# Optimization experiments

Measured on AMD Instinct MI355X. Metric: run time of the kernel, lower is better.

The kernel has to match this reference:

```python
import jax, jax.numpy as jnp
import numpy as np

R_CUT = 10.0  # init arg r_cut


def _per_mol(pos, T, eneg, node_attrs, an, q_tot, eidx, hardness, cov_radii):
    # pos [N,3], T [N,E], eneg [N], node_attrs [N,num_el], an [N] int,
    # q_tot scalar, eidx [2,E] int
    N = pos.shape[0]
    E = T.shape[1]
    dtype = pos.dtype
    sqrt_pi = jnp.sqrt(jnp.pi).astype(dtype)
    sqrt_2 = jnp.sqrt(2.0).astype(dtype)
    eye = jnp.eye(N, dtype=dtype)
    # pairwise distances; +eye makes the (masked-out) diagonal sqrt-safe
    diff = pos[:, None, :] - pos[None, :, :]
    d = jnp.sqrt(jnp.sum(diff * diff, axis=-1) + eye)  # [N,N]
    r = cov_radii[an]                                   # [N]
    sigma = r * r
    gamma = jnp.sqrt(sigma[:, None] + sigma[None, :])   # [N,N]
    diag_vals = hardness[jnp.argmax(node_attrs, axis=-1)] + 1.0 / (sqrt_pi * r)
    A = jax.scipy.special.erf(d / (sqrt_2 * gamma)) / d * (1.0 - eye) + jnp.diag(diag_vals)
    # per-edge cutoff diagonal: 1/cos(pi*r/(2*r_cut)) - 1
    e0, e1 = eidx[0], eidx[1]
    edge_d = jnp.sqrt(jnp.sum((pos[e0] - pos[e1]) ** 2, axis=-1))  # [E]
    cut = 1.0 / jnp.cos(jnp.pi * edge_d / (2.0 * R_CUT)) - 1.0
    Ap = T.T @ A @ T + jnp.diag(cut)                    # [E,E]
    # augment with charge-conservation row/col of ones
    ones_col = jnp.ones((E, 1), dtype=dtype)
    ones_row = jnp.ones((1, E + 1), dtype=dtype)
    Aaug = jnp.concatenate([jnp.concatenate([Ap, ones_col], axis=1), ones_row], axis=0)
    b = jnp.concatenate([-(T.T @ eneg), q_tot[None]])   # [E+1]
    x = jnp.linalg.solve(Aaug, b)[:-1]                  # [E] split charges
    return T @ x                                        # [N] atomic partial charges


def setup_inputs() -> dict:
    key = jax.random.key(0)
    B, N, E, NUM_EL, NZ = 256, 64, 512, 10, 119
    ks = jax.random.split(key, 10)
    positions = jax.random.normal(ks[0], (B, N, 3), dtype=jnp.float32)
    T = jax.random.normal(ks[1], (B, N, E), dtype=jnp.float32)
    eneg = jax.random.normal(ks[2], (B, N), dtype=jnp.float32)
    node_attrs = jax.random.normal(ks[3], (B, N, NUM_EL), dtype=jnp.float32)
    total_charge = jax.random.normal(ks[4], (B,), dtype=jnp.float32)
    atomic_numbers = jax.random.randint(ks[5], (B, N), 1, 100)
    e0 = jax.random.randint(ks[6], (B, E), 0, N)
    off = jax.random.randint(ks[7], (B, E), 1, N)
    edge_index = jnp.stack([e0, (e0 + off) % N], axis=1)  # [B,2,E], distinct endpoints
    hardness = jax.random.uniform(ks[8], (NUM_EL,), dtype=jnp.float32)
    cov_radii = 0.3 + 2.2 * jax.random.uniform(ks[9], (NZ,), dtype=jnp.float32)
    p = jnp.zeros((1,), dtype=jnp.float32)  # only used for .device in torch
    return dict(positions=positions, T=T, eneg=eneg, node_attrs=node_attrs,
                total_charge=total_charge, p=p, hardness=hardness,
                cov_radii=cov_radii, atomic_numbers=atomic_numbers,
                edge_index=edge_index)


def reference(positions, T, eneg, node_attrs, total_charge, p, hardness,
              cov_radii, atomic_numbers, edge_index):
    charges = jax.vmap(_per_mol, in_axes=(0, 0, 0, 0, 0, 0, 0, None, None))(
        positions, T, eneg, node_attrs, atomic_numbers, total_charge,
        edge_index, hardness, cov_radii)  # [B,N]
    return charges.reshape(-1)  # concat over molecules, as in the torch loop
```

## Files before the change

kernel.cpp:

```cpp
#include <hip/hip_runtime.h>
#include <math.h>

#define SQRT_PI 1.7724538509055160273
#define SQRT_2  1.4142135623730950488
#define PI_OVER_2RC 0.15707963267948966
#define W0 32.0

typedef double dbl4 __attribute__((ext_vector_type(4)));


__device__ __forceinline__ double bcast64(double v, int lane) {
    union { double d; unsigned int u[2]; } a, r;
    a.d = v;
    r.u[0] = __builtin_amdgcn_readlane(a.u[0], lane);
    r.u[1] = __builtin_amdgcn_readlane(a.u[1], lane);
    return r.d;
}

__device__ __forceinline__ double a_entry(int i, int j, const double* posd,
                                          const double* sig, const double* dg) {
    if (i == j) return dg[i];
    double dx = posd[3*i+0]-posd[3*j+0];
    double dy = posd[3*i+1]-posd[3*j+1];
    double dz = posd[3*i+2]-posd[3*j+2];
    double d  = sqrt(dx*dx+dy*dy+dz*dz);
    double g  = sqrt(sig[i]+sig[j]);
    return erf(d/(SQRT_2*g))/d;
}

__device__ __forceinline__ dbl4 mfma64(int cS, double xv, double yv, dbl4 acc) {
    return cS ? __builtin_amdgcn_mfma_f64_16x16x4f64(yv, xv, acc, 0, 0, 0)
              : __builtin_amdgcn_mfma_f64_16x16x4f64(xv, yv, acc, 0, 0, 0);
}

__global__ __launch_bounds__(64)
void k0_probe(double* __restrict__ fl)
{
    const int l = threadIdx.x;
    const int kl = l >> 4, ml = l & 15;
    const double af1 = (double)(l + 1),  bf1 = (double)(l + 65);
    const double af2 = (double)(1 + ((l*7 + 3) % 61));
    const double bf2 = (double)(2 + ((l*13 + 5) % 53));
    dbl4 c1 = {0.0,0.0,0.0,0.0}, c2 = {0.0,0.0,0.0,0.0};
    c1 = __builtin_amdgcn_mfma_f64_16x16x4f64(af1, bf1, c1, 0, 0, 0);
    c2 = __builtin_amdgcn_mfma_f64_16x16x4f64(af2, bf2, c2, 0, 0, 0);
    int best = -1;
    for (int h = 0; h < 32; ++h) {
        if (best >= 0) break;
        const int cS = h >> 4, cA = (h >> 3) & 1, cB = (h >> 2) & 1, cD = h & 3;
        bool ok = true;
        #pragma unroll
        for (int r = 0; r < 4; ++r) {
            int row, col;
            const int v0 = 4*kl + r, v1 = kl + 4*r;
            if (cD == 0)      { row = v0; col = ml; }
            else if (cD == 1) { row = v1; col = ml; }
            else if (cD == 2) { row = ml; col = v0; }
            else              { row = ml; col = v1; }
            double r1 = 0.0, r2 = 0.0;
            #pragma unroll
            for (int k = 0; k < 4; ++k) {
                const int la = cA ? (row*4 + k) : (row + 16*k);
                const int lb = cB ? (col*4 + k) : (col + 16*k);
                if (cS == 0) {
                    r1 += (double)(la + 1) * (double)(lb + 65);
                    r2 += (double)(1 + ((la*7+3) % 61)) * (double)(2 + ((lb*13+5) % 53));
                } else {
                    r1 += (double)(lb + 1) * (double)(la + 65);
                    r2 += (double)(1 + ((lb*7+3) % 61)) * (double)(2 + ((la*13+5) % 53));
                }
            }
            if (c1[r] != r1 || c2[r] != r2) ok = false;
        }
        if (__ballot(ok) == ~0ull) best = h;
    }
    if (l == 0) {
        fl[0] = (best >= 0) ? 1.0 : 0.0;
        fl[1] = (double)((best >= 0) ? (best >> 4)      : 0);
        fl[2] = (double)((best >= 0) ? ((best >> 3) & 1) : 0);
        fl[3] = (double)((best >= 0) ? ((best >> 2) & 1) : 0);
        fl[4] = (double)((best >= 0) ? (best & 3)        : 0);
    }
}

__global__ __launch_bounds__(256, 2)
void k1_gram(const float* __restrict__ pos, const float* __restrict__ T,
             const int* __restrict__ eidx, double* __restrict__ ws)
{
    const int bx = blockIdx.x;
    const int m = bx >> 1, s = bx & 1;
    const int Bm = gridDim.x >> 1;
    const int tid = threadIdx.x;
    const int wid = tid >> 6, l = tid & 63;
    const int kl = l >> 4, ml = l & 15;

    __shared__ float  Tch[64*68];
    __shared__ double posd[192];
    __shared__ double w_sl[256];
    __shared__ float  sw32[256];
    __shared__ double ptb[4][64];
    __shared__ unsigned long long fmask[4];

    const float* Tm = T + (size_t)m*64*512;
    const double* flq = ws + (size_t)Bm*8322;
    const int useM = (flq[0] != 0.0);
    const int cS = (int)flq[1], cA = (int)flq[2], cB = (int)flq[3], cD = (int)flq[4];
    const int aRow = cA ? (l >> 2) : ml;
    const int aK   = cA ? (l & 3)  : kl;
    const int bRow = cB ? (l >> 2) : ml;
    const int bK   = cB ? (l & 3)  : kl;
    int drow[4], dcol[4];
    #pragma unroll
    for (int r = 0; r < 4; ++r) {
        const int v0 = 4*kl + r, v1 = kl + 4*r;
        if (cD == 0)      { drow[r] = v0; dcol[r] = ml; }
        else if (cD == 1) { drow[r] = v1; dcol[r] = ml; }
        else if (cD == 2) { drow[r] = ml; dcol[r] = v0; }
        else              { drow[r] = ml; dcol[r] = v1; }
    }

    if (tid < 64) {
        posd[3*tid+0] = (double)pos[(m*64+tid)*3+0];
        posd[3*tid+1] = (double)pos[(m*64+tid)*3+1];
        posd[3*tid+2] = (double)pos[(m*64+tid)*3+2];
    }
    __syncthreads();

    {
        const int e = s*256 + tid;
        const int a0 = eidx[(size_t)m*1024 + e];
        const int a1 = eidx[(size_t)m*1024 + 512 + e];
        double dx = posd[3*a0+0]-posd[3*a1+0];
        double dy = posd[3*a0+1]-posd[3*a1+1];
        double dz = posd[3*a0+2]-posd[3*a1+2];
        double d  = sqrt(dx*dx+dy*dy+dz*dz);
        double w  = 1.0 / (1.0/cos(PI_OVER_2RC*d) - 1.0);
        w_sl[tid] = w;
        sw32[tid] = (w > W0) ? 0.0f : (float)sqrt(w);
    }
    __syncthreads();
    if (tid < 64) {
        #pragma unroll
        for (int c2 = 0; c2 < 4; ++c2) {
            unsigned long long mk = __ballot(w_sl[c2*64 + tid] > W0);
            if (tid == 0) fmask[c2] = mk;
        }
    }

    const int si = tid & 15, sj = tid >> 4;
    const int ti64 = tid & 63, tg = tid >> 6;

    const unsigned int enc = (wid==0) ? 0x020100u :
                             (wid==1) ? 0x121103u :
                             (wid==2) ? 0xFF2213u : 0xFF3323u;
    dbl4 vacc[3];
    #pragma unroll
    for (int t = 0; t < 3; ++t) vacc[t] = (dbl4){0.0, 0.0, 0.0, 0.0};

    const int PP_[10] = {0,0,0,0,1,1,1,2,2,3};
    const int QQ_[10] = {0,1,2,3,1,2,3,2,3,3};
    double acc64[10];
    float  a32[10];
    #pragma unroll
    for (int k = 0; k < 10; ++k) { acc64[k] = 0.0; a32[k] = 0.0f; }
    double t0b_p = 0.0;

    for (int cc = 0; cc < 4; ++cc) {
        const int gch = s*4 + cc;
        __syncthreads();
        #pragma unroll
        for (int k = 0; k < 4; ++k) {
            int ll = tid + 256*k, row = ll >> 4, c4 = (ll & 15)*4;
            float4 v = *(const float4*)&Tm[row*512 + gch*64 + c4];
            *(float4*)&Tch[row*68 + c4] = v;
        }
        __syncthreads();
        #pragma unroll
        for (int k = 0; k < 16; ++k) {
            int e = tg*16 + k;
            double tv = (double)Tch[ti64*68 + e];
            t0b_p += tv * w_sl[cc*64 + e];
        }
        if (useM) {
            for (int kk = 0; kk < 16; ++kk) {
                const double wB = w_sl[cc*64 + 4*kk + bK];
                #pragma unroll
                for (int t = 0; t < 3; ++t) {
                    const unsigned int pq = (enc >> (8*t)) & 0xFFu;
                    if (pq != 0xFFu) {
                        const int p = pq >> 4, q = pq & 15;
                        double xv = (double)Tch[(p*16 + aRow)*68 + 4*kk + aK];
                        double yv = wB * (double)Tch[(q*16 + bRow)*68 + 4*kk + bK];
                        vacc[t] = mfma64(cS, xv, yv, vacc[t]);
                    }
                }
            }
        } else {
            {
                unsigned long long mm = fmask[cc];
                while (mm) {
                    int e = __builtin_ctzll(mm); mm &= mm - 1;
                    double we = w_sl[cc*64 + e];
                    double ad[4], bd[4];
                    #pragma unroll
                    for (int p = 0; p < 4; ++p) ad[p] = (double)Tch[(si+16*p)*68 + e];
                    #pragma unroll
                    for (int q = 0; q < 4; ++q) bd[q] = we * (double)Tch[(sj+16*q)*68 + e];
                    #pragma unroll
                    for (int k = 0; k < 10; ++k) acc64[k] += ad[PP_[k]] * bd[QQ_[k]];
                }
            }
            __syncthreads();
            #pragma unroll
            for (int k = 0; k < 4; ++k) {
                int ll = tid + 256*k, row = ll >> 4, c4 = (ll & 15)*4;
                float4 v = *(float4*)&Tch[row*68 + c4];
                v.x *= sw32[cc*64 + c4+0];
                v.y *= sw32[cc*64 + c4+1];
                v.z *= sw32[cc*64 + c4+2];
                v.w *= sw32[cc*64 + c4+3];
                *(float4*)&Tch[row*68 + c4] = v;
            }
            __syncthreads();
            #pragma unroll
            for (int e4 = 0; e4 < 16; ++e4) {
                float4 av4[4], bv4[4];
                #pragma unroll
                for (int p = 0; p < 4; ++p) av4[p] = *(float4*)&Tch[(si+16*p)*68 + e4*4];
                #pragma unroll
                for (int q = 0; q < 4; ++q) bv4[q] = *(float4*)&Tch[(sj+16*q)*68 + e4*4];
                #pragma unroll
                for (int k = 0; k < 10; ++k) {
                    const float4 a4 = av4[PP_[k]], b4 = bv4[QQ_[k]];
                    a32[k] += a4.x*b4.x + a4.y*b4.y + a4.z*b4.z + a4.w*b4.w;
                }
                if ((e4 & 3) == 3) {
                    #pragma unroll
                    for (int k = 0; k < 10; ++k) { acc64[k] += (double)a32[k]; a32[k] = 0.0f; }
                }
            }
        }
    }
    __syncthreads();

    double* Sp = ws + ((size_t)(s*Bm + m))*4096;
    if (useM) {
        #pragma unroll
        for (int t = 0; t < 3; ++t) {
            const unsigned int pq = (enc >> (8*t)) & 0xFFu;
            if (pq != 0xFFu) {
                const int p = pq >> 4, q = pq & 15;
                #pragma unroll
                for (int r = 0; r < 4; ++r) {
                    Sp[(p*16 + drow[r])*64 + q*16 + dcol[r]] = vacc[t][r];
                    if (p != q)
                        Sp[(q*16 + dcol[r])*64 + p*16 + drow[r]] = vacc[t][r];
                }
            }
        }
    } else {
        #pragma unroll
        for (int k = 0; k < 10; ++k) {
            int i = si + 16*PP_[k], j = sj + 16*QQ_[k];
            Sp[i*64 + j] = acc64[k];
            if (PP_[k] != QQ_[k]) Sp[j*64 + i] = acc64[k];
        }
    }

    ptb[tg][ti64] = t0b_p;
    __syncthreads();
    if (tid < 64) {
        double* t0q = ws + (size_t)2*Bm*4096;
        t0q[(size_t)(s*Bm + m)*64 + tid] =
            ptb[0][tid]+ptb[1][tid]+ptb[2][tid]+ptb[3][tid];
        double sw = w_sl[tid] + w_sl[64+tid] + w_sl[128+tid] + w_sl[192+tid];
        #pragma unroll
        for (int off = 32; off > 0; off >>= 1) sw += __shfl_down(sw, off);
        if (tid == 0) {
            double* swq = ws + (size_t)2*Bm*4096 + (size_t)2*Bm*64;
            swq[s*Bm + m] = sw;
        }
    }
}

__global__ __launch_bounds__(1024)
void k2_solve(const float* __restrict__ pos, const float* __restrict__ nattr,
              const float* __restrict__ eneg, const float* __restrict__ qtot,
              const float* __restrict__ hard, const float* __restrict__ covr,
              const int* __restrict__ an, double* __restrict__ ws,
              float* __restrict__ outp)
{
    const int m = blockIdx.x, tid = threadIdx.x;
    const int Bm = gridDim.x;
    const int jl = tid & 63;
    const int rg = tid >> 6;
    const int kl = jl >> 4, ml = jl & 15;

    __shared__ double AB[64*65];
    __shared__ double PB[64*33];
    __shared__ double posd[192], sig_s[64], dg_s[64], eneg_s[64];
    __shared__ double t0a_s[64], t0b_s[64], ga_s[64], gb_s[64], ua_s[64], ub_s[64];
    __shared__ double sa_s[64], sb_s[64];
    __shared__ double dinv_s[64], dvec_s[64];
    __shared__ double lam_sh;

    const double* Sp0 = ws + (size_t)m*4096;
    const double* Sp1 = ws + (size_t)(Bm + m)*4096;
    const double* t0q = ws + (size_t)2*Bm*4096;
    const double* swq = t0q + (size_t)2*Bm*64;
    const double* flq = ws + (size_t)Bm*8322;

    const int useM = (flq[0] != 0.0);
    const int cS = (int)flq[1], cA = (int)flq[2], cB = (int)flq[3], cD = (int)flq[4];
    const int aRow = cA ? (jl >> 2) : ml;
    const int aK   = cA ? (jl & 3)  : kl;
    const int bRow = cB ? (jl >> 2) : ml;
    const int bK   = cB ? (jl & 3)  : kl;
    int drow[4], dcol[4];
    #pragma unroll
    for (int r = 0; r < 4; ++r) {
        const int v0 = 4*kl + r, v1 = kl + 4*r;
        if (cD == 0)      { drow[r] = v0; dcol[r] = ml; }
        else if (cD == 1) { drow[r] = v1; dcol[r] = ml; }
        else if (cD == 2) { drow[r] = ml; dcol[r] = v0; }
        else              { drow[r] = ml; dcol[r] = v1; }
    }

    double sreg[4];
    #pragma unroll
    for (int kk = 0; kk < 4; ++kk)
        sreg[kk] = Sp0[4*tid + kk] + Sp1[4*tid + kk];

    if (tid < 64) {
        posd[3*tid+0] = (double)pos[(m*64+tid)*3+0];
        posd[3*tid+1] = (double)pos[(m*64+tid)*3+1];
        posd[3*tid+2] = (double)pos[(m*64+tid)*3+2];
        double r = (double)covr[an[m*64+tid]];
        sig_s[tid] = r*r;
        const float* np_ = nattr + (size_t)(m*64+tid)*10;
        float best = np_[0]; int bi = 0;
        #pragma unroll
        for (int k = 1; k < 10; ++k) { float v = np_[k]; if (v > best) { best = v; bi = k; } }
        dg_s[tid] = (double)hard[bi] + 1.0/(SQRT_PI*r);
    } else if (tid < 128) {
        int ll = tid - 64;
        t0b_s[ll] = t0q[(size_t)m*64 + ll] + t0q[(size_t)(Bm+m)*64 + ll];
    } else if (tid < 192) {
        int ll = tid - 128;
        eneg_s[ll] = (double)eneg[m*64 + ll];
    }
    __syncthreads();

    double areg[4];
    #pragma unroll
    for (int p = 0; p < 4; ++p) {
        int i = rg + 16*p;
        double v = a_entry(i, jl, posd, sig_s, dg_s);
        areg[p] = v;
        AB[i*65 + jl] = v;
    }
    {
        const int c16 = tid & 15, row16 = tid >> 4;
        double a = 0.0;
        #pragma unroll
        for (int kk = 0; kk < 4; ++kk) a += sreg[kk] * eneg_s[4*c16 + kk];
        a += __shfl_down(a, 8, 16);
        a += __shfl_down(a, 4, 16);
        a += __shfl_down(a, 2, 16);
        a += __shfl_down(a, 1, 16);
        if (c16 == 0) t0a_s[row16] = -a;
    }
    __syncthreads();

    {
        double ra[4], rb[4];
        const double ta = t0a_s[jl], tb = t0b_s[jl];
        #pragma unroll
        for (int p = 0; p < 4; ++p) { ra[p] = areg[p]*ta; rb[p] = areg[p]*tb; }
        #pragma unroll
        for (int off = 32; off > 0; off >>= 1) {
            #pragma unroll
            for (int p = 0; p < 4; ++p) {
                ra[p] += __shfl_down(ra[p], off);
                rb[p] += __shfl_down(rb[p], off);
            }
        }
        if (jl == 0) {
            #pragma unroll
            for (int p = 0; p < 4; ++p) { ga_s[rg+16*p] = ra[p]; gb_s[rg+16*p] = rb[p]; }
        }
    }
    __syncthreads();

    if (useM) {
        const int ti1 = rg >> 2;
        const int tjp = (rg & 3) >> 1;
        const int kh  = rg & 1;
        const int ti2 = rg >> 2, tj2 = rg & 3;
        dbl4 macc;
        #pragma unroll
        for (int r = 0; r < 4; ++r)
            macc[r] = AB[(ti2*16 + drow[r])*65 + tj2*16 + dcol[r]];
        for (int pass = 0; pass < 2; ++pass) {
            const int kbase = pass*32;
            dbl4 pacc = {0.0, 0.0, 0.0, 0.0};
            #pragma unroll
            for (int kk = 0; kk < 8; ++kk) {
                const int kg = kh*8 + kk;
                double xv = AB[(ti1*16 + aRow)*65 + 4*kg + aK];
                size_t so = (size_t)(4*kg + bK)*64 + kbase + tjp*16 + bRow;
                double yv = Sp0[so] + Sp1[so];
                pacc = mfma64(cS, xv, yv, pacc);
            }
            __syncthreads();
            if (kh == 0) {
                #pragma unroll
                for (int r = 0; r < 4; ++r)
                    PB[(ti1*16 + drow[r])*33 + tjp*16 + dcol[r]] = pacc[r];
            }
            __syncthreads();
            if (kh == 1) {
                #pragma unroll
                for (int r = 0; r < 4; ++r)
                    PB[(ti1*16 + drow[r])*33 + tjp*16 + dcol[r]] += pacc[r];
            }
            __syncthreads();
            #pragma unroll
            for (int kk = 0; kk < 8; ++kk) {
                double xv = PB[(ti2*16 + aRow)*33 + 4*kk + aK];
                double yv = AB[(kbase + 4*kk + bK)*65 + tj2*16 + bRow];
                macc = mfma64(cS, xv, yv, macc);
            }
        }
        __syncthreads();
        #pragma unroll
        for (int r = 0; r < 4; ++r)
            AB[(ti2*16 + drow[r])*65 + tj2*16 + dcol[r]] = macc[r];
        __syncthreads();
    } else {
        double macc[4];
        #pragma unroll
        for (int p = 0; p < 4; ++p) macc[p] = areg[p];
        for (int pass = 0; pass < 2; ++pass) {
            const int kbase = pass*32;
            __syncthreads();
            for (int l2 = tid; l2 < 2048; l2 += 1024) {
                int c = l2 >> 6, k = l2 & 63;
                PB[c*64 + k] = Sp0[(size_t)(kbase+c)*64 + k] + Sp1[(size_t)(kbase+c)*64 + k];
            }
            __syncthreads();
            const int c0 = 2*rg, c1 = c0 + 1;
            double p0 = 0.0, p1 = 0.0;
            #pragma unroll 4
            for (int k = 0; k < 64; ++k) {
                double a = AB[jl*65 + k];
                p0 += a * PB[c0*64 + k];
                p1 += a * PB[c1*64 + k];
            }
            __syncthreads();
            PB[jl*33 + c0] = p0;
            PB[jl*33 + c1] = p1;
            __syncthreads();
            #pragma unroll 4
            for (int cl = 0; cl < 32; ++cl) {
                double lb = AB[(kbase+cl)*65 + jl];
                #pragma unroll
                for (int p = 0; p < 4; ++p)
                    macc[p] += PB[(rg+16*p)*33 + cl] * lb;
            }
        }
        __syncthreads();
        #pragma unroll
        for (int p = 0; p < 4; ++p) AB[(rg+16*p)*65 + jl] = macc[p];
        __syncthreads();
    }

    for (int pb = 0; pb < 4; ++pb) {
        const int kb = pb*16;
        if (tid < 64) {
            const int i = tid;
            double pr[16];
            #pragma unroll
            for (int c = 0; c < 16; ++c) pr[c] = AB[i*65 + kb + c];
            #pragma unroll
            for (int c = 0; c < 16; ++c) {
                const int k = kb + c;
                const double Dk = bcast64(pr[c], k);
                const double di = 1.0 / Dk;
                if (i == k) { dinv_s[k] = di; dvec_s[k] = Dk; }
                const double lik = pr[c] * di;
                #pragma unroll
                for (int j = c+1; j < 16; ++j) {
                    const double mkj = bcast64(pr[j], k);
                    if (i > k) pr[j] -= lik * mkj;
                }
                if (i > k) pr[c] = lik;
            }
            #pragma unroll
            for (int c = 0; c < 16; ++c) AB[i*65 + kb + c] = pr[c];
        }
        __syncthreads();
        const int lim = kb + 16;
        if (lim < 64) {
            double tacc[4] = {0.0, 0.0, 0.0, 0.0};
            #pragma unroll 4
            for (int c = 0; c < 16; ++c) {
                double lbv = AB[jl*65 + kb + c] * dvec_s[kb + c];
                #pragma unroll
                for (int p = 0; p < 4; ++p)
                    tacc[p] += AB[(rg+16*p)*65 + kb + c] * lbv;
            }
            if (jl >= lim) {
                #pragma unroll
                for (int p = 0; p < 4; ++p) {
                    int i = rg + 16*p;
                    if (i >= lim) AB[i*65 + jl] -= tacc[p];
                }
            }
        }
        __syncthreads();
    }

    if (tid < 64) {
        const int i = tid;
        double ha = ga_s[i], hb = gb_s[i];
        #pragma unroll
        for (int j = 0; j < 63; ++j) {
            double xa = bcast64(ha, j), xb = bcast64(hb, j);
            double lij = (i > j) ? AB[i*65+j] : 0.0;
            ha -= lij*xa; hb -= lij*xb;
        }
        double di = dinv_s[i];
        ha *= di; hb *= di;
        #pragma unroll
        for (int j = 63; j > 0; --j) {
            double xa = bcast64(ha, j), xb = bcast64(hb, j);
            double lji = (i < j) ? AB[j*65+i] : 0.0;
            ha -= lji*xa; hb -= lji*xb;
        }
        ua_s[i] = ha; ub_s[i] = hb;
    }
    __syncthreads();

    {
        double ra[4], rb[4];
        const double uaj = ua_s[jl], ubj = ub_s[jl];
        #pragma unroll
        for (int p = 0; p < 4; ++p) { ra[p] = areg[p]*uaj; rb[p] = areg[p]*ubj; }
        #pragma unroll
        for (int off = 32; off > 0; off >>= 1) {
            #pragma unroll
            for (int p = 0; p < 4; ++p) {
                ra[p] += __shfl_down(ra[p], off);
                rb[p] += __shfl_down(rb[p], off);
            }
        }
        if (jl == 0) {
            #pragma unroll
            for (int p = 0; p < 4; ++p) {
                sa_s[rg + 16*p] = ra[p];
                sb_s[rg + 16*p] = rb[p];
            }
        }
    }
    __syncthreads();

    {
        const int c16 = tid & 15, row16 = tid >> 4;
        double q1 = 0.0, q2 = 0.0;
        #pragma unroll
        for (int kk = 0; kk < 4; ++kk) {
            q1 += sreg[kk] * sa_s[4*c16 + kk];
            q2 += sreg[kk] * sb_s[4*c16 + kk];
        }
        q1 += __shfl_down(q1, 8, 16); q2 += __shfl_down(q2, 8, 16);
        q1 += __shfl_down(q1, 4, 16); q2 += __shfl_down(q2, 4, 16);
        q1 += __shfl_down(q1, 2, 16); q2 += __shfl_down(q2, 2, 16);
        q1 += __shfl_down(q1, 1, 16); q2 += __shfl_down(q2, 1, 16);
        if (c16 == 0) { PB[row16] = q1; PB[64 + row16] = q2; }
    }
    if (tid < 64) {
        double d1 = (eneg_s[tid] + sa_s[tid]) * t0b_s[tid];
        double d2 = sb_s[tid] * t0b_s[tid];
        #pragma unroll
        for (int off = 32; off > 0; off >>= 1) {
            d1 += __shfl_down(d1, off);
            d2 += __shfl_down(d2, off);
        }
        if (tid == 0) {
            double sw1 = swq[m] + swq[Bm + m];
            double sY = -d1;
            double sZ = sw1 - d2;
            lam_sh = ((double)qtot[m] - sY) / (1.0 - sZ);
        }
    }
    __syncthreads();
    if (tid < 64) {
        double p1 = t0a_s[tid] - PB[tid];
        double p2 = t0b_s[tid] - PB[64 + tid];
        outp[m*64 + tid] = (float)(p1 - lam_sh*p2);
    }
}

extern "C" void kernel_launch(void* const* d_in, const int* in_sizes, int n_in,
                              void* d_out, int out_size, void* d_ws, size_t ws_size,
                              hipStream_t stream) {
    const float* pos  = (const float*)d_in[0];
    const float* T    = (const float*)d_in[1];
    const float* eneg = (const float*)d_in[2];
    const float* nat  = (const float*)d_in[3];
    const float* qt   = (const float*)d_in[4];
    const float* hard = (const float*)d_in[6];
    const float* covr = (const float*)d_in[7];
    const int*   an   = (const int*)d_in[8];
    const int*   eidx = (const int*)d_in[9];
    float* outp = (float*)d_out;
    (void)n_in; (void)out_size; (void)ws_size;

    const int B = in_sizes[4];
    double* ws = (double*)d_ws;

    k0_probe<<<dim3(1), dim3(64), 0, stream>>>(ws + (size_t)B*8322);
    k1_gram<<<dim3(2*B), dim3(256), 0, stream>>>(pos, T, eidx, ws);
    k2_solve<<<dim3(B), dim3(1024), 0, stream>>>(pos, nat, eneg, qt, hard,
                                                 covr, an, ws, outp);
}
```

Measured before the change: 181.3 us.

## Fuse Gram kernel into solve kernel, keeping the weighted Gram matrix in LDS

Result: slower. 195.6 us (+7.9%).

```diff
diff --git a/kernel.cpp b/kernel.cpp
--- a/kernel.cpp
+++ b/kernel.cpp
@@ -4,7 +4,6 @@
 #define SQRT_PI 1.7724538509055160273
 #define SQRT_2  1.4142135623730950488
 #define PI_OVER_2RC 0.15707963267948966
-#define W0 32.0
 
 typedef double dbl4 __attribute__((ext_vector_type(4)));
 
@@ -83,234 +82,31 @@
     }
 }
 
-__global__ __launch_bounds__(256, 2)
-void k1_gram(const float* __restrict__ pos, const float* __restrict__ T,
-             const int* __restrict__ eidx, double* __restrict__ ws)
-{
-    const int bx = blockIdx.x;
-    const int m = bx >> 1, s = bx & 1;
-    const int Bm = gridDim.x >> 1;
-    const int tid = threadIdx.x;
-    const int wid = tid >> 6, l = tid & 63;
-    const int kl = l >> 4, ml = l & 15;
-
-    __shared__ float  Tch[64*68];
-    __shared__ double posd[192];
-    __shared__ double w_sl[256];
-    __shared__ float  sw32[256];
-    __shared__ double ptb[4][64];
-    __shared__ unsigned long long fmask[4];
-
-    const float* Tm = T + (size_t)m*64*512;
-    const double* flq = ws + (size_t)Bm*8322;
-    const int useM = (flq[0] != 0.0);
-    const int cS = (int)flq[1], cA = (int)flq[2], cB = (int)flq[3], cD = (int)flq[4];
-    const int aRow = cA ? (l >> 2) : ml;
-    const int aK   = cA ? (l & 3)  : kl;
-    const int bRow = cB ? (l >> 2) : ml;
-    const int bK   = cB ? (l & 3)  : kl;
-    int drow[4], dcol[4];
-    #pragma unroll
-    for (int r = 0; r < 4; ++r) {
-        const int v0 = 4*kl + r, v1 = kl + 4*r;
-        if (cD == 0)      { drow[r] = v0; dcol[r] = ml; }
-        else if (cD == 1) { drow[r] = v1; dcol[r] = ml; }
-        else if (cD == 2) { drow[r] = ml; dcol[r] = v0; }
-        else              { drow[r] = ml; dcol[r] = v1; }
-    }
-
-    if (tid < 64) {
-        posd[3*tid+0] = (double)pos[(m*64+tid)*3+0];
-        posd[3*tid+1] = (double)pos[(m*64+tid)*3+1];
-        posd[3*tid+2] = (double)pos[(m*64+tid)*3+2];
-    }
-    __syncthreads();
-
-    {
-        const int e = s*256 + tid;
-        const int a0 = eidx[(size_t)m*1024 + e];
-        const int a1 = eidx[(size_t)m*1024 + 512 + e];
-        double dx = posd[3*a0+0]-posd[3*a1+0];
-        double dy = posd[3*a0+1]-posd[3*a1+1];
-        double dz = posd[3*a0+2]-posd[3*a1+2];
-        double d  = sqrt(dx*dx+dy*dy+dz*dz);
-        double w  = 1.0 / (1.0/cos(PI_OVER_2RC*d) - 1.0);
-        w_sl[tid] = w;
-        sw32[tid] = (w > W0) ? 0.0f : (float)sqrt(w);
-    }
-    __syncthreads();
-    if (tid < 64) {
-        #pragma unroll
-        for (int c2 = 0; c2 < 4; ++c2) {
-            unsigned long long mk = __ballot(w_sl[c2*64 + tid] > W0);
-            if (tid == 0) fmask[c2] = mk;
-        }
-    }
-
-    const int si = tid & 15, sj = tid >> 4;
-    const int ti64 = tid & 63, tg = tid >> 6;
-
-    const unsigned int enc = (wid==0) ? 0x020100u :
-                             (wid==1) ? 0x121103u :
-                             (wid==2) ? 0xFF2213u : 0xFF3323u;
-    dbl4 vacc[3];
-    #pragma unroll
-    for (int t = 0; t < 3; ++t) vacc[t] = (dbl4){0.0, 0.0, 0.0, 0.0};
-
-    const int PP_[10] = {0,0,0,0,1,1,1,2,2,3};
-    const int QQ_[10] = {0,1,2,3,1,2,3,2,3,3};
-    double acc64[10];
-    float  a32[10];
-    #pragma unroll
-    for (int k = 0; k < 10; ++k) { acc64[k] = 0.0; a32[k] = 0.0f; }
-    double t0b_p = 0.0;
-
-    for (int cc = 0; cc < 4; ++cc) {
-        const int gch = s*4 + cc;
-        __syncthreads();
-        #pragma unroll
-        for (int k = 0; k < 4; ++k) {
-            int ll = tid + 256*k, row = ll >> 4, c4 = (ll & 15)*4;
-            float4 v = *(const float4*)&Tm[row*512 + gch*64 + c4];
-            *(float4*)&Tch[row*68 + c4] = v;
-        }
-        __syncthreads();
-        #pragma unroll
-        for (int k = 0; k < 16; ++k) {
-            int e = tg*16 + k;
-            double tv = (double)Tch[ti64*68 + e];
-            t0b_p += tv * w_sl[cc*64 + e];
-        }
-        if (useM) {
-            for (int kk = 0; kk < 16; ++kk) {
-                const double wB = w_sl[cc*64 + 4*kk + bK];
-                #pragma unroll
-                for (int t = 0; t < 3; ++t) {
-                    const unsigned int pq = (enc >> (8*t)) & 0xFFu;
-                    if (pq != 0xFFu) {
-                        const int p = pq >> 4, q = pq & 15;
-                        double xv = (double)Tch[(p*16 + aRow)*68 + 4*kk + aK];
-                        double yv = wB * (double)Tch[(q*16 + bRow)*68 + 4*kk + bK];
-                        vacc[t] = mfma64(cS, xv, yv, vacc[t]);
-                    }
-                }
-            }
-        } else {
-            {
-                unsigned long long mm = fmask[cc];
-                while (mm) {
-                    int e = __builtin_ctzll(mm); mm &= mm - 1;
-                    double we = w_sl[cc*64 + e];
-                    double ad[4], bd[4];
-                    #pragma unroll
-                    for (int p = 0; p < 4; ++p) ad[p] = (double)Tch[(si+16*p)*68 + e];
-                    #pragma unroll
-                    for (int q = 0; q < 4; ++q) bd[q] = we * (double)Tch[(sj+16*q)*68 + e];
-                    #pragma unroll
-                    for (int k = 0; k < 10; ++k) acc64[k] += ad[PP_[k]] * bd[QQ_[k]];
-                }
-            }
-            __syncthreads();
-            #pragma unroll
-            for (int k = 0; k < 4; ++k) {
-                int ll = tid + 256*k, row = ll >> 4, c4 = (ll & 15)*4;
-                float4 v = *(float4*)&Tch[row*68 + c4];
-                v.x *= sw32[cc*64 + c4+0];
-                v.y *= sw32[cc*64 + c4+1];
-                v.z *= sw32[cc*64 + c4+2];
-                v.w *= sw32[cc*64 + c4+3];
-                *(float4*)&Tch[row*68 + c4] = v;
-            }
-            __syncthreads();
-            #pragma unroll
-            for (int e4 = 0; e4 < 16; ++e4) {
-                float4 av4[4], bv4[4];
-                #pragma unroll
-                for (int p = 0; p < 4; ++p) av4[p] = *(float4*)&Tch[(si+16*p)*68 + e4*4];
-                #pragma unroll
-                for (int q = 0; q < 4; ++q) bv4[q] = *(float4*)&Tch[(sj+16*q)*68 + e4*4];
-                #pragma unroll
-                for (int k = 0; k < 10; ++k) {
-                    const float4 a4 = av4[PP_[k]], b4 = bv4[QQ_[k]];
-                    a32[k] += a4.x*b4.x + a4.y*b4.y + a4.z*b4.z + a4.w*b4.w;
-                }
-                if ((e4 & 3) == 3) {
-                    #pragma unroll
-                    for (int k = 0; k < 10; ++k) { acc64[k] += (double)a32[k]; a32[k] = 0.0f; }
-                }
-            }
-        }
-    }
-    __syncthreads();
-
-    double* Sp = ws + ((size_t)(s*Bm + m))*4096;
-    if (useM) {
-        #pragma unroll
-        for (int t = 0; t < 3; ++t) {
-            const unsigned int pq = (enc >> (8*t)) & 0xFFu;
-            if (pq != 0xFFu) {
-                const int p = pq >> 4, q = pq & 15;
-                #pragma unroll
-                for (int r = 0; r < 4; ++r) {
-                    Sp[(p*16 + drow[r])*64 + q*16 + dcol[r]] = vacc[t][r];
-                    if (p != q)
-                        Sp[(q*16 + dcol[r])*64 + p*16 + drow[r]] = vacc[t][r];
-                }
-            }
-        }
-    } else {
-        #pragma unroll
-        for (int k = 0; k < 10; ++k) {
-            int i = si + 16*PP_[k], j = sj + 16*QQ_[k];
-            Sp[i*64 + j] = acc64[k];
-            if (PP_[k] != QQ_[k]) Sp[j*64 + i] = acc64[k];
-        }
-    }
-
-    ptb[tg][ti64] = t0b_p;
-    __syncthreads();
-    if (tid < 64) {
-        double* t0q = ws + (size_t)2*Bm*4096;
-        t0q[(size_t)(s*Bm + m)*64 + tid] =
-            ptb[0][tid]+ptb[1][tid]+ptb[2][tid]+ptb[3][tid];
-        double sw = w_sl[tid] + w_sl[64+tid] + w_sl[128+tid] + w_sl[192+tid];
-        #pragma unroll
-        for (int off = 32; off > 0; off >>= 1) sw += __shfl_down(sw, off);
-        if (tid == 0) {
-            double* swq = ws + (size_t)2*Bm*4096 + (size_t)2*Bm*64;
-            swq[s*Bm + m] = sw;
-        }
-    }
-}
-
 __global__ __launch_bounds__(1024)
-void k2_solve(const float* __restrict__ pos, const float* __restrict__ nattr,
-              const float* __restrict__ eneg, const float* __restrict__ qtot,
-              const float* __restrict__ hard, const float* __restrict__ covr,
-              const int* __restrict__ an, double* __restrict__ ws,
-              float* __restrict__ outp)
+void k_fused(const float* __restrict__ pos, const float* __restrict__ T,
+             const int* __restrict__ eidx, const float* __restrict__ nattr,
+             const float* __restrict__ eneg, const float* __restrict__ qtot,
+             const float* __restrict__ hard, const float* __restrict__ covr,
+             const int* __restrict__ an, const double* __restrict__ flq,
+             float* __restrict__ outp)
 {
     const int m = blockIdx.x, tid = threadIdx.x;
-    const int Bm = gridDim.x;
     const int jl = tid & 63;
     const int rg = tid >> 6;
     const int kl = jl >> 4, ml = jl & 15;
 
     __shared__ double AB[64*65];
-    __shared__ double PB[64*33];
+    __shared__ double SB[64*65];
+    __shared__ union {
+        struct { float Tch[64*68]; double w_sl[512]; } g;
+        double PF[64*65];
+    } U;
     __shared__ double posd[192], sig_s[64], dg_s[64], eneg_s[64];
-    __shared__ double t0a_s[64], t0b_s[64], ga_s[64], gb_s[64], ua_s[64], ub_s[64];
-    __shared__ double sa_s[64], sb_s[64];
+    __shared__ double t0a_s[64], t0b_s[64], ga_s[64], gb_s[64];
+    __shared__ double ua_s[64], ub_s[64], sa_s[64], sb_s[64];
     __shared__ double dinv_s[64], dvec_s[64];
-    __shared__ double lam_sh;
-
-    const double* Sp0 = ws + (size_t)m*4096;
-    const double* Sp1 = ws + (size_t)(Bm + m)*4096;
-    const double* t0q = ws + (size_t)2*Bm*4096;
-    const double* swq = t0q + (size_t)2*Bm*64;
-    const double* flq = ws + (size_t)Bm*8322;
-
-    const int useM = (flq[0] != 0.0);
+    __shared__ double lam_sh, sw_sh;
+
     const int cS = (int)flq[1], cA = (int)flq[2], cB = (int)flq[3], cD = (int)flq[4];
     const int aRow = cA ? (jl >> 2) : ml;
     const int aK   = cA ? (jl & 3)  : kl;
@@ -326,11 +122,6 @@
         else              { drow[r] = ml; dcol[r] = v1; }
     }
 
-    double sreg[4];
-    #pragma unroll
-    for (int kk = 0; kk < 4; ++kk)
-        sreg[kk] = Sp0[4*tid + kk] + Sp1[4*tid + kk];
-
     if (tid < 64) {
         posd[3*tid+0] = (double)pos[(m*64+tid)*3+0];
         posd[3*tid+1] = (double)pos[(m*64+tid)*3+1];
@@ -344,13 +135,19 @@
         dg_s[tid] = (double)hard[bi] + 1.0/(SQRT_PI*r);
     } else if (tid < 128) {
         int ll = tid - 64;
-        t0b_s[ll] = t0q[(size_t)m*64 + ll] + t0q[(size_t)(Bm+m)*64 + ll];
-    } else if (tid < 192) {
-        int ll = tid - 128;
         eneg_s[ll] = (double)eneg[m*64 + ll];
     }
     __syncthreads();
 
+    if (tid < 512) {
+        const int a0 = eidx[(size_t)m*1024 + tid];
+        const int a1 = eidx[(size_t)m*1024 + 512 + tid];
+        double dx = posd[3*a0+0]-posd[3*a1+0];
+        double dy = posd[3*a0+1]-posd[3*a1+1];
+        double dz = posd[3*a0+2]-posd[3*a1+2];
+        double d  = sqrt(dx*dx+dy*dy+dz*dz);
+        U.g.w_sl[tid] = 1.0 / (1.0/cos(PI_OVER_2RC*d) - 1.0);
+    }
     double areg[4];
     #pragma unroll
     for (int p = 0; p < 4; ++p) {
@@ -359,11 +156,82 @@
         areg[p] = v;
         AB[i*65 + jl] = v;
     }
+    __syncthreads();
+
+    if (tid < 64) {
+        double s = 0.0;
+        #pragma unroll
+        for (int c = 0; c < 8; ++c) s += U.g.w_sl[c*64 + tid];
+        #pragma unroll
+        for (int off = 32; off > 0; off >>= 1) s += __shfl_down(s, off);
+        if (tid == 0) sw_sh = s;
+    }
+
+    const int TP_[10] = {0,1,1,2,2,2,3,3,3,3};
+    const int TQ_[10] = {0,0,1,0,1,2,0,1,2,3};
+    const int myt = (rg < 10) ? rg : rg - 10;
+    const int tp = TP_[myt], tq = TQ_[myt];
+    dbl4 vacc = {0.0, 0.0, 0.0, 0.0};
+    double t0b_p = 0.0;
+    const int srow = tid >> 4, sc4 = (tid & 15) * 4;
+    const float* Tm = T + (size_t)m*64*512;
+
+    for (int cc = 0; cc < 8; ++cc) {
+        __syncthreads();
+        float4 v = *(const float4*)&Tm[srow*512 + cc*64 + sc4];
+        *(float4*)&U.g.Tch[srow*68 + sc4] = v;
+        t0b_p += (double)v.x * U.g.w_sl[cc*64 + sc4+0]
+               + (double)v.y * U.g.w_sl[cc*64 + sc4+1]
+               + (double)v.z * U.g.w_sl[cc*64 + sc4+2]
+               + (double)v.w * U.g.w_sl[cc*64 + sc4+3];
+        __syncthreads();
+        const bool doit = (rg >= 6 && rg < 10) ||
+                          (rg < 6 ? ((cc & 1) == 0) : ((cc & 1) == 1));
+        if (doit) {
+            #pragma unroll
+            for (int kk = 0; kk < 16; ++kk) {
+                const double wB = U.g.w_sl[cc*64 + 4*kk + bK];
+                double xv = (double)U.g.Tch[(tp*16 + aRow)*68 + 4*kk + aK];
+                double yv = wB * (double)U.g.Tch[(tq*16 + bRow)*68 + 4*kk + bK];
+                vacc = mfma64(cS, xv, yv, vacc);
+            }
+        }
+    }
+
+    if (rg < 10) {
+        #pragma unroll
+        for (int r = 0; r < 4; ++r) {
+            const int ri = tp*16 + drow[r], cj = tq*16 + dcol[r];
+            SB[ri*65 + cj] = vacc[r];
+            if (tp != tq) SB[cj*65 + ri] = vacc[r];
+        }
+    }
+    {
+        double t = t0b_p;
+        t += __shfl_down(t, 8, 16);
+        t += __shfl_down(t, 4, 16);
+        t += __shfl_down(t, 2, 16);
+        t += __shfl_down(t, 1, 16);
+        if ((tid & 15) == 0) t0b_s[tid >> 4] = t;
+    }
+    __syncthreads();
+    if (rg >= 10) {
+        #pragma unroll
+        for (int r = 0; r < 4; ++r) {
+            const int ri = tp*16 + drow[r], cj = tq*16 + dcol[r];
+            double v = vacc[r];
+            SB[ri*65 + cj] += v;
+            if (tp != tq) SB[cj*65 + ri] += v;
+        }
+    }
+    __syncthreads();
+
     {
         const int c16 = tid & 15, row16 = tid >> 4;
         double a = 0.0;
         #pragma unroll
-        for (int kk = 0; kk < 4; ++kk) a += sreg[kk] * eneg_s[4*c16 + kk];
+        for (int kk = 0; kk < 4; ++kk)
+            a += SB[row16*65 + 4*c16 + kk] * eneg_s[4*c16 + kk];
         a += __shfl_down(a, 8, 16);
         a += __shfl_down(a, 4, 16);
         a += __shfl_down(a, 2, 16);
@@ -392,88 +260,38 @@
     }
     __syncthreads();
 
-    if (useM) {
-        const int ti1 = rg >> 2;
-        const int tjp = (rg & 3) >> 1;
-        const int kh  = rg & 1;
-        const int ti2 = rg >> 2, tj2 = rg & 3;
+    const int ti = rg >> 2, tj = rg & 3;
+    {
+        dbl4 pacc = {0.0, 0.0, 0.0, 0.0};
+        #pragma unroll
+        for (int kk = 0; kk < 16; ++kk) {
+            double xv = AB[(ti*16 + aRow)*65 + 4*kk + aK];
+            double yv = SB[(4*kk + bK)*65 + tj*16 + bRow];
+            pacc = mfma64(cS, xv, yv, pacc);
+        }
+        #pragma unroll
+        for (int r = 0; r < 4; ++r)
+            U.PF[(ti*16 + drow[r])*65 + tj*16 + dcol[r]] = pacc[r];
+    }
+    __syncthreads();
+
+    {
         dbl4 macc;
         #pragma unroll
         for (int r = 0; r < 4; ++r)
-            macc[r] = AB[(ti2*16 + drow[r])*65 + tj2*16 + dcol[r]];
-        for (int pass = 0; pass < 2; ++pass) {
-            const int kbase = pass*32;
-            dbl4 pacc = {0.0, 0.0, 0.0, 0.0};
-            #pragma unroll
-            for (int kk = 0; kk < 8; ++kk) {
-                const int kg = kh*8 + kk;
-                double xv = AB[(ti1*16 + aRow)*65 + 4*kg + aK];
-                size_t so = (size_t)(4*kg + bK)*64 + kbase + tjp*16 + bRow;
-                double yv = Sp0[so] + Sp1[so];
-                pacc = mfma64(cS, xv, yv, pacc);
-            }
-            __syncthreads();
-            if (kh == 0) {
-                #pragma unroll
-                for (int r = 0; r < 4; ++r)
-                    PB[(ti1*16 + drow[r])*33 + tjp*16 + dcol[r]] = pacc[r];
-            }
-            __syncthreads();
-            if (kh == 1) {
-                #pragma unroll
-                for (int r = 0; r < 4; ++r)
-                    PB[(ti1*16 + drow[r])*33 + tjp*16 + dcol[r]] += pacc[r];
-            }
-            __syncthreads();
-            #pragma unroll
-            for (int kk = 0; kk < 8; ++kk) {
-                double xv = PB[(ti2*16 + aRow)*33 + 4*kk + aK];
-                double yv = AB[(kbase + 4*kk + bK)*65 + tj2*16 + bRow];
-                macc = mfma64(cS, xv, yv, macc);
-            }
+            macc[r] = AB[(ti*16 + drow[r])*65 + tj*16 + dcol[r]];
+        #pragma unroll
+        for (int kk = 0; kk < 16; ++kk) {
+            double xv = U.PF[(ti*16 + aRow)*65 + 4*kk + aK];
+            double yv = AB[(4*kk + bK)*65 + tj*16 + bRow];
+            macc = mfma64(cS, xv, yv, macc);
         }
         __syncthreads();
         #pragma unroll
         for (int r = 0; r < 4; ++r)
-            AB[(ti2*16 + drow[r])*65 + tj2*16 + dcol[r]] = macc[r];
-        __syncthreads();
-    } else {
-        double macc[4];
-        #pragma unroll
-        for (int p = 0; p < 4; ++p) macc[p] = areg[p];
-        for (int pass = 0; pass < 2; ++pass) {
-            const int kbase = pass*32;
-            __syncthreads();
-            for (int l2 = tid; l2 < 2048; l2 += 1024) {
-                int c = l2 >> 6, k = l2 & 63;
-                PB[c*64 + k] = Sp0[(size_t)(kbase+c)*64 + k] + Sp1[(size_t)(kbase+c)*64 + k];
-            }
-            __syncthreads();
-            const int c0 = 2*rg, c1 = c0 + 1;
-            double p0 = 0.0, p1 = 0.0;
-            #pragma unroll 4
-            for (int k = 0; k < 64; ++k) {
-                double a = AB[jl*65 + k];
-                p0 += a * PB[c0*64 + k];
-                p1 += a * PB[c1*64 + k];
-            }
-            __syncthreads();
-            PB[jl*33 + c0] = p0;
-            PB[jl*33 + c1] = p1;
-            __syncthreads();
-            #pragma unroll 4
-            for (int cl = 0; cl < 32; ++cl) {
-                double lb = AB[(kbase+cl)*65 + jl];
-                #pragma unroll
-                for (int p = 0; p < 4; ++p)
-                    macc[p] += PB[(rg+16*p)*33 + cl] * lb;
-            }
-        }
-        __syncthreads();
-        #pragma unroll
-        for (int p = 0; p < 4; ++p) AB[(rg+16*p)*65 + jl] = macc[p];
-        __syncthreads();
-    }
+            AB[(ti*16 + drow[r])*65 + tj*16 + dcol[r]] = macc[r];
+    }
+    __syncthreads();
 
     for (int pb = 0; pb < 4; ++pb) {
         const int kb = pb*16;
@@ -570,14 +388,15 @@
         double q1 = 0.0, q2 = 0.0;
         #pragma unroll
         for (int kk = 0; kk < 4; ++kk) {
-            q1 += sreg[kk] * sa_s[4*c16 + kk];
-            q2 += sreg[kk] * sb_s[4*c16 + kk];
+            const double sv = SB[row16*65 + 4*c16 + kk];
+            q1 += sv * sa_s[4*c16 + kk];
+            q2 += sv * sb_s[4*c16 + kk];
         }
         q1 += __shfl_down(q1, 8, 16); q2 += __shfl_down(q2, 8, 16);
         q1 += __shfl_down(q1, 4, 16); q2 += __shfl_down(q2, 4, 16);
         q1 += __shfl_down(q1, 2, 16); q2 += __shfl_down(q2, 2, 16);
         q1 += __shfl_down(q1, 1, 16); q2 += __shfl_down(q2, 1, 16);
-        if (c16 == 0) { PB[row16] = q1; PB[64 + row16] = q2; }
+        if (c16 == 0) { U.PF[row16] = q1; U.PF[64 + row16] = q2; }
     }
     if (tid < 64) {
         double d1 = (eneg_s[tid] + sa_s[tid]) * t0b_s[tid];
@@ -588,16 +407,15 @@
             d2 += __shfl_down(d2, off);
         }
         if (tid == 0) {
-            double sw1 = swq[m] + swq[Bm + m];
             double sY = -d1;
-            double sZ = sw1 - d2;
+            double sZ = sw_sh - d2;
             lam_sh = ((double)qtot[m] - sY) / (1.0 - sZ);
         }
     }
     __syncthreads();
     if (tid < 64) {
-        double p1 = t0a_s[tid] - PB[tid];
-        double p2 = t0b_s[tid] - PB[64 + tid];
+        double p1 = t0a_s[tid] - U.PF[tid];
+        double p2 = t0b_s[tid] - U.PF[64 + tid];
         outp[m*64 + tid] = (float)(p1 - lam_sh*p2);
     }
 }
@@ -620,8 +438,7 @@
     const int B = in_sizes[4];
     double* ws = (double*)d_ws;
 
-    k0_probe<<<dim3(1), dim3(64), 0, stream>>>(ws + (size_t)B*8322);
-    k1_gram<<<dim3(2*B), dim3(256), 0, stream>>>(pos, T, eidx, ws);
-    k2_solve<<<dim3(B), dim3(1024), 0, stream>>>(pos, nat, eneg, qt, hard,
-                                                 covr, an, ws, outp);
-}
+    k0_probe<<<dim3(1), dim3(64), 0, stream>>>(ws);
+    k_fused<<<dim3(B), dim3(1024), 0, stream>>>(pos, T, eidx, nat, eneg, qt,
+                                                hard, covr, an, ws, outp);
+}
```
